# Kernel optimization log

Measured on AMD Instinct MI355X. Metric: run time of the kernel, lower is better.

The kernel has to match this reference:

```python
import jax, jax.numpy as jnp
import numpy as np
from jax.scipy.linalg import expm

D_LOGIC = 128
D_MEM = 16
SO_DIM = D_MEM * (D_MEM - 1) // 2  # 120


def _linear_init(key, fan_in, shape):
    bound = 1.0 / np.sqrt(fan_in)
    return jax.random.uniform(key, shape, jnp.float32, -bound, bound)


def setup_inputs() -> dict:
    key = jax.random.key(0)
    ks = jax.random.split(key, 14)
    B, S = 4, 128
    return {
        "x_logic": jax.random.normal(ks[0], (B, S, D_LOGIC), jnp.float32),
        "x_memory": jax.random.normal(ks[1], (B, S, D_MEM), jnp.float32),
        # W_Q / W_K
        "Wq": _linear_init(ks[2], D_LOGIC, (D_LOGIC, D_LOGIC)),
        "bq": _linear_init(ks[3], D_LOGIC, (D_LOGIC,)),
        "Wk": _linear_init(ks[4], D_LOGIC, (D_LOGIC, D_LOGIC)),
        "bk": _linear_init(ks[5], D_LOGIC, (D_LOGIC,)),
        # gamma_net: Linear(d_logic, 2*d_logic) -> Tanh -> Linear(2*d_logic, so_dim)
        "W1": _linear_init(ks[6], D_LOGIC, (2 * D_LOGIC, D_LOGIC)),
        "b1": _linear_init(ks[7], D_LOGIC, (2 * D_LOGIC,)),
        "W2": _linear_init(ks[8], 2 * D_LOGIC, (SO_DIM, 2 * D_LOGIC)),
        "b2": _linear_init(ks[9], 2 * D_LOGIC, (SO_DIM,)),
        # out_proj: Linear(d_memory, d_memory)
        "Wo": _linear_init(ks[10], D_MEM, (D_MEM, D_MEM)),
        "bo": _linear_init(ks[11], D_MEM, (D_MEM,)),
    }


def reference(x_logic, x_memory, Wq, bq, Wk, bk, W1, b1, W2, b2, Wo, bo):
    B, S, d_logic = x_logic.shape
    dm = x_memory.shape[-1]

    # attention over logic stream
    Q = x_logic @ Wq.T + bq
    K = x_logic @ Wk.T + bk
    attn = jax.nn.softmax(
        jnp.einsum("bjd,bid->bji", Q, K) / jnp.sqrt(jnp.float32(d_logic)), axis=-1
    )  # [B, S(j), S(i)]

    # per-pair Lie-algebra params: delta[b,j,i] = x_logic[b,j] - x_logic[b,i]
    delta = x_logic[:, :, None, :] - x_logic[:, None, :, :]  # [B,S,S,d_logic]
    h = jnp.tanh(delta @ W1.T + b1)
    lie = h @ W2.T + b2  # [B,S,S,so_dim]

    # scatter into skew-symmetric matrices [B,S,S,dm,dm]
    r, c = np.triu_indices(dm, k=1)
    skew = jnp.zeros((B, S, S, dm, dm), x_logic.dtype)
    skew = skew.at[..., r, c].set(lie)
    skew = skew.at[..., c, r].set(-lie)

    # Lie-group exponential -> orthogonal transport matrices
    T_all = expm(skew)  # [B,S,S,dm,dm]

    # transported[b,j,i,:] = T[b,j,i] @ x_memory[b,i]
    transported = jnp.einsum("bjide,bie->bjid", T_all, x_memory)

    # attention-weighted aggregation over i
    settled = jnp.einsum("bji,bjid->bjd", attn, transported)  # [B,S,dm]

    out = settled @ Wo.T + bo
    return out, T_all
```

## Files before the change

### kernel.cpp

```cpp
#include <hip/hip_runtime.h>
#include <hip/hip_fp16.h>

#define S_LEN 128
#define DLOG  128
#define DMEM  16
#define SO    120
#define HDIM  256

typedef _Float16 v8h __attribute__((ext_vector_type(8)));
typedef __fp16 v2hf __attribute__((ext_vector_type(2)));
typedef float v4f __attribute__((ext_vector_type(4)));

union PkU { v2hf h; unsigned u; };
union V8U { v8h v; int u[4]; };

__global__ __launch_bounds__(128) void qk_kernel(
    const float* __restrict__ xl, const float* __restrict__ Wq,
    const float* __restrict__ bq, const float* __restrict__ Wk,
    const float* __restrict__ bk, float* __restrict__ Q, float* __restrict__ K) {
  int bj = blockIdx.x, o = threadIdx.x;
  __shared__ float xs[128];
  xs[o] = xl[bj * 128 + o];
  __syncthreads();
  float aq = bq[o], ak = bk[o];
  const float* wq = Wq + o * 128;
  const float* wk = Wk + o * 128;
  #pragma unroll 4
  for (int d = 0; d < 128; ++d) {
    float x = xs[d];
    aq = fmaf(x, wq[d], aq);
    ak = fmaf(x, wk[d], ak);
  }
  Q[bj * 128 + o] = aq;
  K[bj * 128 + o] = ak;
}

__global__ __launch_bounds__(128) void attn_kernel(
    const float* __restrict__ Q, const float* __restrict__ K,
    float* __restrict__ attn) {
  int bj = blockIdx.x, b = bj >> 7, i = threadIdx.x;
  __shared__ float qs[128];
  __shared__ float red[128];
  qs[i] = Q[bj * 128 + i];
  __syncthreads();
  const float* kr = K + (b * 128 + i) * 128;
  float s = 0.f;
  #pragma unroll 4
  for (int d = 0; d < 128; ++d) s = fmaf(qs[d], kr[d], s);
  s *= 0.08838834764831845f;
  red[i] = s;
  __syncthreads();
  for (int off = 64; off; off >>= 1) {
    if (i < off) red[i] = fmaxf(red[i], red[i + off]);
    __syncthreads();
  }
  float m = red[0];
  __syncthreads();
  float e = expf(s - m);
  red[i] = e;
  __syncthreads();
  for (int off = 64; off; off >>= 1) {
    if (i < off) red[i] += red[i + off];
    __syncthreads();
  }
  attn[(size_t)bj * 128 + i] = e / red[0];
}

__global__ __launch_bounds__(256) void h_kernel(
    const float* __restrict__ xl, const float* __restrict__ W1,
    const float* __restrict__ b1, __half* __restrict__ hG) {
  __shared__ _Float16 w1s[128 * 136];
  __shared__ _Float16 dstage[64 * 136];
  __shared__ float xjs[128];
  int t = threadIdx.x;
  int blk = blockIdx.x;
  int bj = blk >> 1;
  int oh = blk & 1;
  int b = bj >> 7;
  int o0 = oh * 128;

  if (t < 128) xjs[t] = xl[bj * 128 + t];
  for (int idx = t; idx < 128 * 128; idx += 256) {
    int o = idx >> 7, k = idx & 127;
    w1s[o * 136 + k] = (_Float16)W1[(o0 + o) * 128 + k];
  }
  __syncthreads();

  int lane = t & 63, w = t >> 6;
  int nn = lane & 15, q = lane >> 4;
  int ow = o0 + w * 32;
  float bb0 = b1[ow + nn], bb1 = b1[ow + 16 + nn];
  const float* xb = xl + (size_t)b * 128 * 128;

  for (int pi = 0; pi < 2; ++pi) {
    for (int idx = t; idx < 64 * 128; idx += 256) {
      int i = idx >> 7, k = idx & 127;
      dstage[i * 136 + k] = (_Float16)(xjs[k] - xb[(pi * 64 + i) * 128 + k]);
    }
    __syncthreads();

    v4f acc[4][2];
    #pragma unroll
    for (int mi = 0; mi < 4; ++mi) {
      acc[mi][0] = (v4f){0.f, 0.f, 0.f, 0.f};
      acc[mi][1] = (v4f){0.f, 0.f, 0.f, 0.f};
    }
    #pragma unroll
    for (int ks = 0; ks < 4; ++ks) {
      v8h bf0 = *(const v8h*)&w1s[(w * 32 + nn) * 136 + ks * 32 + q * 8];
      v8h bf1 = *(const v8h*)&w1s[(w * 32 + 16 + nn) * 136 + ks * 32 + q * 8];
      #pragma unroll
      for (int mi = 0; mi < 4; ++mi) {
        v8h af = *(const v8h*)&dstage[(mi * 16 + nn) * 136 + ks * 32 + q * 8];
        acc[mi][0] = __builtin_amdgcn_mfma_f32_16x16x32_f16(af, bf0, acc[mi][0], 0, 0, 0);
        acc[mi][1] = __builtin_amdgcn_mfma_f32_16x16x32_f16(af, bf1, acc[mi][1], 0, 0, 0);
      }
    }
    #pragma unroll
    for (int mi = 0; mi < 4; ++mi) {
      #pragma unroll
      for (int nt = 0; nt < 2; ++nt) {
        int o = ow + nt * 16 + nn;
        float bbv = nt ? bb1 : bb0;
        #pragma unroll
        for (int reg = 0; reg < 4; ++reg) {
          int i = pi * 64 + mi * 16 + 4 * q + reg;
          float x = acc[mi][nt][reg] + bbv;
          float ax = fabsf(x);
          float e = __expf(-2.f * ax);
          float r = __fdividef(1.f - e, 1.f + e);
          r = copysignf(r, x);
          hG[(size_t)(bj * 128 + i) * 512 + o] = __float2half(r);
        }
      }
    }
    __syncthreads();
  }
}

__global__ __launch_bounds__(256) void lie_kernel(
    const float* __restrict__ W2g, const float* __restrict__ b2g,
    float* __restrict__ Tg) {
  __shared__ _Float16 w2t[128 * 136];
  int t = threadIdx.x, lane = t & 63;
  int wu = __builtin_amdgcn_readfirstlane(t >> 6);
  int pbase = blockIdx.x * 64 + wu * 16;
  int nn = lane & 15, q = lane >> 4;
  const _Float16* hf = (const _Float16*)Tg;

  v4f acc[8];
  #pragma unroll
  for (int tt = 0; tt < 8; ++tt) acc[tt] = (v4f){0.f, 0.f, 0.f, 0.f};

  const _Float16* hrow = hf + (size_t)(pbase + nn) * 512;
  for (int khalf = 0; khalf < 2; ++khalf) {
    __syncthreads();
    for (int idx = t; idx < 120 * 128; idx += 256) {
      int o = idx >> 7, kk = idx & 127;
      w2t[o * 136 + kk] = (_Float16)W2g[o * 256 + khalf * 128 + kk];
    }
    for (int idx = t; idx < 8 * 128; idx += 256)
      w2t[(120 + (idx >> 7)) * 136 + (idx & 127)] = (_Float16)0.f;
    __syncthreads();
    #pragma unroll
    for (int ks = 0; ks < 4; ++ks) {
      v8h ah = *(const v8h*)(hrow + khalf * 128 + ks * 32 + 8 * q);
      #pragma unroll
      for (int tt = 0; tt < 8; ++tt) {
        const v8h bf = *(const v8h*)(w2t + (16 * tt + nn) * 136 + ks * 32 + 8 * q);
        acc[tt] = __builtin_amdgcn_mfma_f32_16x16x32_f16(ah, bf, acc[tt], 0, 0, 0);
      }
    }
  }

  _Float16* hw = (_Float16*)Tg;
  #pragma unroll
  for (int tt = 0; tt < 8; ++tt) {
    int n16 = 16 * tt + nn;
    if (n16 < 120) {
      float bb = b2g[n16];
      #pragma unroll
      for (int reg = 0; reg < 4; ++reg) {
        size_t p = (size_t)(pbase + 4 * q + reg);
        hw[p * 512 + 256 + n16] = (_Float16)(acc[tt][reg] + bb);
      }
    }
  }
}

__device__ __forceinline__ void split8(const float* x, v8h& hi, v8h& lo) {
  union U { v8h v; v2hf p[4]; } H, L;
  #pragma unroll
  for (int i = 0; i < 4; ++i) {
    float a = x[2 * i], b = x[2 * i + 1];
    v2hf h = __builtin_amdgcn_cvt_pkrtz(a, b);
    float ra = (float)h[0], rb = (float)h[1];
    v2hf l = __builtin_amdgcn_cvt_pkrtz(a - ra, b - rb);
    H.p[i] = h;
    L.p[i] = l;
  }
  hi = H.v;
  lo = L.v;
}

__device__ __forceinline__ int lie_idx(int rr, int cc) {
  return 15 * rr - ((rr * (rr - 1)) >> 1) + cc - rr - 1;
}

__global__ __launch_bounds__(256) void expm_kernel(float* __restrict__ Tg) {
  __shared__ char lds[12288] __attribute__((aligned(16)));
  int t = threadIdx.x, lane = t & 63;
  int wu = __builtin_amdgcn_readfirstlane(t >> 6);
  int pbase = blockIdx.x * 8 + wu * 2;
  int nn = lane & 15, q = lane >> 4, b8 = (q & 1) * 8;
  char* wb = lds + wu * 3072;
  _Float16* lieS = (_Float16*)wb;
  float* ErB = (float*)(wb + 512);
  const _Float16* hf = (const _Float16*)Tg;

  int idxA = ((2 * (q & 1)) * 16 + nn) * 4;
  int idxB = idxA + 64;

  float scv[2];
  int sv[2];
  #pragma unroll
  for (int j = 0; j < 2; ++j) {
    size_t p = (size_t)(pbase + j);
    _Float16 a0 = (lane < 120) ? hf[p * 512 + 256 + lane] : (_Float16)0.f;
    _Float16 a1 = (lane < 56) ? hf[p * 512 + 320 + lane] : (_Float16)0.f;
    lieS[j * 128 + lane] = a0;
    lieS[j * 128 + 64 + lane] = a1;
    float f0 = (float)a0, f1 = (float)a1;
    float s2 = f0 * f0 + f1 * f1;
    #pragma unroll
    for (int off = 1; off < 64; off <<= 1) s2 += __shfl_xor(s2, off, 64);
    float bound = sqrtf(s2);
    int s = 0;
    while (bound > 1.0f && s < 12) { bound *= 0.5f; s++; }
    sv[j] = __builtin_amdgcn_readfirstlane(s);
    scv[j] = ldexpf(1.0f, -s);
  }
  asm volatile("s_waitcnt lgkmcnt(0)" ::: "memory");

  V8U Apk[2], bf[2];
  v4f E[2];
  #pragma unroll
  for (int j = 0; j < 2; ++j) {
    const _Float16* lp = lieS + j * 128;
    float sc = scv[j];
    float av[8];
    #pragma unroll
    for (int jj = 0; jj < 8; ++jj) {
      int c = b8 + jj;
      int rr = min(nn, c), c2 = max(nn, c);
      float lv = (c == nn) ? 0.f : (float)lp[lie_idx(rr, c2)];
      av[jj] = (c == nn) ? 0.f : ((c > nn) ? lv : -lv) * sc;
    }
    #pragma unroll
    for (int i = 0; i < 4; ++i) {
      PkU u;
      u.h = __builtin_amdgcn_cvt_pkrtz(av[2 * i], av[2 * i + 1]);
      Apk[j].u[i] = (int)u.u;
    }
    #pragma unroll
    for (int i = 0; i < 4; ++i) bf[j].u[i] = Apk[j].u[i] ^ 0x80008000;
    #pragma unroll
    for (int reg = 0; reg < 4; ++reg) {
      int r = 4 * q + reg;
      int rr = min(r, nn), c2 = max(r, nn);
      float lv = (r == nn) ? 0.f : (float)lp[lie_idx(rr, c2)];
      float v = (r == nn) ? 0.f : ((nn > r) ? lv : -lv) * sc;
      E[j][reg] = v + ((r == nn) ? 1.f : 0.f);
    }
  }

  #pragma unroll
  for (int k = 2; k <= 9; ++k) {
    const float rk = 1.0f / (2.0f * (float)k);
    #pragma unroll
    for (int j = 0; j < 2; ++j) {
      v4f z = {0.f, 0.f, 0.f, 0.f};
      v4f c4 = __builtin_amdgcn_mfma_f32_16x16x32_f16(Apk[j].v, bf[j].v, z, 0, 0, 0);
      c4 = c4 * rk;
      E[j] += c4;
      if (k < 9) {
        PkU u0, u1;
        u0.h = __builtin_amdgcn_cvt_pkrtz(c4[0], c4[1]);
        u1.h = __builtin_amdgcn_cvt_pkrtz(c4[2], c4[3]);
        bf[j].u[0] = __builtin_amdgcn_ds_bpermute(idxA, (int)u0.u);
        bf[j].u[1] = __builtin_amdgcn_ds_bpermute(idxA, (int)u1.u);
        bf[j].u[2] = __builtin_amdgcn_ds_bpermute(idxB, (int)u0.u);
        bf[j].u[3] = __builtin_amdgcn_ds_bpermute(idxB, (int)u1.u);
      }
    }
  }

  int smax = max(sv[0], sv[1]);
  for (int it = 0; it < smax; ++it) {
    #pragma unroll
    for (int j = 0; j < 2; ++j) {
      if (it < sv[j]) {
        float* Erp = ErB + j * 320;
        PkU u0, u1;
        u0.h = __builtin_amdgcn_cvt_pkrtz(E[j][0], E[j][1]);
        u1.h = __builtin_amdgcn_cvt_pkrtz(E[j][2], E[j][3]);
        V8U bfe;
        bfe.u[0] = __builtin_amdgcn_ds_bpermute(idxA, (int)u0.u);
        bfe.u[1] = __builtin_amdgcn_ds_bpermute(idxA, (int)u1.u);
        bfe.u[2] = __builtin_amdgcn_ds_bpermute(idxB, (int)u0.u);
        bfe.u[3] = __builtin_amdgcn_ds_bpermute(idxB, (int)u1.u);
        #pragma unroll
        for (int reg = 0; reg < 4; ++reg)
          Erp[(4 * q + reg) * 20 + nn] = E[j][reg];
        asm volatile("s_waitcnt lgkmcnt(0)" ::: "memory");
        float4 a0 = *(const float4*)(Erp + nn * 20 + b8);
        float4 a1 = *(const float4*)(Erp + nn * 20 + b8 + 4);
        float xa[8] = {a0.x, a0.y, a0.z, a0.w, a1.x, a1.y, a1.z, a1.w};
        v8h ahi, alo;
        split8(xa, ahi, alo);
        v8h Ecat = (q < 2) ? ahi : alo;
        v4f z = {0.f, 0.f, 0.f, 0.f};
        E[j] = __builtin_amdgcn_mfma_f32_16x16x32_f16(Ecat, bfe.v, z, 0, 0, 0);
      }
    }
  }

  #pragma unroll
  for (int j = 0; j < 2; ++j) {
    float* dst = Tg + (size_t)(pbase + j) * 256;
    #pragma unroll
    for (int reg = 0; reg < 4; ++reg)
      dst[(4 * q + reg) * 16 + nn] = E[j][reg];
  }
}

__global__ __launch_bounds__(256) void settle_kernel(
    const float* __restrict__ Tg, const float* __restrict__ attn,
    const float* __restrict__ xm, const float* __restrict__ Wo,
    const float* __restrict__ bo, float* __restrict__ outp) {
  int bj = blockIdx.x, b = bj >> 7;
  int t = threadIdx.x, lane = t & 63;
  int wu = __builtin_amdgcn_readfirstlane(t >> 6);
  int r = lane >> 2, a = lane & 3;
  float pacc = 0.f;
  for (int ii = 0; ii < 32; ++ii) {
    int i = wu * 32 + ii;
    size_t p = (size_t)bj * 128 + i;
    const float4 tv = *(const float4*)(Tg + (p << 8) + lane * 4);
    const float* xv = xm + (b * 128 + i) * 16;
    float aw = attn[p];
    float y = tv.x * xv[4 * a] + tv.y * xv[4 * a + 1] +
              tv.z * xv[4 * a + 2] + tv.w * xv[4 * a + 3];
    y += __shfl_xor(y, 1, 64);
    y += __shfl_xor(y, 2, 64);
    pacc = fmaf(aw, y, pacc);
  }
  __shared__ float sred[4][16];
  __shared__ float sfin[16];
  if (a == 0) sred[wu][r] = pacc;
  __syncthreads();
  if (t < 16) sfin[t] = sred[0][t] + sred[1][t] + sred[2][t] + sred[3][t];
  __syncthreads();
  if (t < 16) {
    float o = bo[t];
    const float* wr = Wo + t * 16;
    #pragma unroll
    for (int c = 0; c < 16; c++) o = fmaf(wr[c], sfin[c], o);
    outp[bj * 16 + t] = o;
  }
}

extern "C" void kernel_launch(void* const* d_in, const int* in_sizes, int n_in,
                              void* d_out, int out_size, void* d_ws,
                              size_t ws_size, hipStream_t stream) {
  const float* xl = (const float*)d_in[0];
  const float* xm = (const float*)d_in[1];
  const float* Wq = (const float*)d_in[2];
  const float* bq = (const float*)d_in[3];
  const float* Wk = (const float*)d_in[4];
  const float* bk = (const float*)d_in[5];
  const float* W1 = (const float*)d_in[6];
  const float* b1 = (const float*)d_in[7];
  const float* W2 = (const float*)d_in[8];
  const float* b2 = (const float*)d_in[9];
  const float* Wo = (const float*)d_in[10];
  const float* bo = (const float*)d_in[11];
  float* outp = (float*)d_out;
  float* Tg = outp + 8192;
  float* wsf = (float*)d_ws;
  float* Q = wsf;
  float* K = wsf + 65536;
  float* attn = wsf + 131072;

  hipLaunchKernelGGL(qk_kernel, dim3(512), dim3(128), 0, stream, xl, Wq, bq, Wk, bk, Q, K);
  hipLaunchKernelGGL(attn_kernel, dim3(512), dim3(128), 0, stream, Q, K, attn);
  hipLaunchKernelGGL(h_kernel, dim3(1024), dim3(256), 0, stream, xl, W1, b1, (__half*)Tg);
  hipLaunchKernelGGL(lie_kernel, dim3(1024), dim3(256), 0, stream, W2, b2, Tg);
  hipLaunchKernelGGL(expm_kernel, dim3(8192), dim3(256), 0, stream, Tg);
  hipLaunchKernelGGL(settle_kernel, dim3(512), dim3(256), 0, stream, Tg, attn, xm, Wo, bo, outp);
}
```

Baseline: 218.6 us.

## Evaluate Taylor expm via Paterson-Stockmeyer and fuse settle reduction into expm

The sequential degree-9 Taylor recurrence (eight dependent MFMAs per pair) becomes a Paterson-Stockmeyer style polynomial built from A, A^2, A^4 and a few combining MFMAs, which shortens the dependent chain. It also exploits A^T = -A by using negated-A fragments. The attention-weighted transport reduction moves from a separate settle kernel that reread all of T into the expm epilogue, which writes per-block partial sums, and a small final kernel applies the output projection. The polynomial coefficients are folded into fp16 operands, which may change numerical accuracy.

```diff
diff --git a/kernel.cpp b/kernel.cpp
--- a/kernel.cpp
+++ b/kernel.cpp
@@ -13,6 +13,12 @@
 
 union PkU { v2hf h; unsigned u; };
 union V8U { v8h v; int u[4]; };
+
+__device__ __forceinline__ v8h splat8(float x) {
+  _Float16 h = (_Float16)x;
+  v8h v = {h, h, h, h, h, h, h, h};
+  return v;
+}
 
 __global__ __launch_bounds__(128) void qk_kernel(
     const float* __restrict__ xl, const float* __restrict__ Wq,
@@ -207,8 +213,11 @@
   return 15 * rr - ((rr * (rr - 1)) >> 1) + cc - rr - 1;
 }
 
-__global__ __launch_bounds__(256) void expm_kernel(float* __restrict__ Tg) {
+__global__ __launch_bounds__(256) void expm_kernel(
+    float* __restrict__ Tg, const float* __restrict__ attn,
+    const float* __restrict__ xm, float* __restrict__ part) {
   __shared__ char lds[12288] __attribute__((aligned(16)));
+  __shared__ float sred[4][16];
   int t = threadIdx.x, lane = t & 63;
   int wu = __builtin_amdgcn_readfirstlane(t >> 6);
   int pbase = blockIdx.x * 8 + wu * 2;
@@ -242,8 +251,8 @@
   }
   asm volatile("s_waitcnt lgkmcnt(0)" ::: "memory");
 
-  V8U Apk[2], bf[2];
-  v4f E[2];
+  V8U Apk[2], BfA[2];
+  v4f Af[2];
   #pragma unroll
   for (int j = 0; j < 2; ++j) {
     const _Float16* lp = lieS + j * 128;
@@ -261,38 +270,107 @@
       PkU u;
       u.h = __builtin_amdgcn_cvt_pkrtz(av[2 * i], av[2 * i + 1]);
       Apk[j].u[i] = (int)u.u;
-    }
-    #pragma unroll
-    for (int i = 0; i < 4; ++i) bf[j].u[i] = Apk[j].u[i] ^ 0x80008000;
+      BfA[j].u[i] = Apk[j].u[i] ^ 0x80008000;
+    }
     #pragma unroll
     for (int reg = 0; reg < 4; ++reg) {
       int r = 4 * q + reg;
       int rr = min(r, nn), c2 = max(r, nn);
       float lv = (r == nn) ? 0.f : (float)lp[lie_idx(rr, c2)];
-      float v = (r == nn) ? 0.f : ((nn > r) ? lv : -lv) * sc;
-      E[j][reg] = v + ((r == nn) ? 1.f : 0.f);
-    }
-  }
-
-  #pragma unroll
-  for (int k = 2; k <= 9; ++k) {
-    const float rk = 1.0f / (2.0f * (float)k);
-    #pragma unroll
-    for (int j = 0; j < 2; ++j) {
-      v4f z = {0.f, 0.f, 0.f, 0.f};
-      v4f c4 = __builtin_amdgcn_mfma_f32_16x16x32_f16(Apk[j].v, bf[j].v, z, 0, 0, 0);
-      c4 = c4 * rk;
-      E[j] += c4;
-      if (k < 9) {
-        PkU u0, u1;
-        u0.h = __builtin_amdgcn_cvt_pkrtz(c4[0], c4[1]);
-        u1.h = __builtin_amdgcn_cvt_pkrtz(c4[2], c4[3]);
-        bf[j].u[0] = __builtin_amdgcn_ds_bpermute(idxA, (int)u0.u);
-        bf[j].u[1] = __builtin_amdgcn_ds_bpermute(idxA, (int)u1.u);
-        bf[j].u[2] = __builtin_amdgcn_ds_bpermute(idxB, (int)u0.u);
-        bf[j].u[3] = __builtin_amdgcn_ds_bpermute(idxB, (int)u1.u);
-      }
-    }
+      Af[j][reg] = (r == nn) ? 0.f : ((nn > r) ? lv : -lv) * sc;
+    }
+  }
+
+  V8U IC1, IC2;
+  #pragma unroll
+  for (int i = 0; i < 4; ++i) {
+    float d0 = (b8 + 2 * i == nn) ? 1.f : 0.f;
+    float d1 = (b8 + 2 * i + 1 == nn) ? 1.f : 0.f;
+    PkU u1, u2;
+    u1.h = __builtin_amdgcn_cvt_pkrtz(10.666667f * d0, 10.666667f * d1);
+    u2.h = __builtin_amdgcn_cvt_pkrtz(2.1333333f * d0, 2.1333333f * d1);
+    IC1.u[i] = (int)u1.u;
+    IC2.u[i] = (int)u2.u;
+  }
+
+  v4f z4 = {0.f, 0.f, 0.f, 0.f};
+
+  v4f cB[2];
+  #pragma unroll
+  for (int j = 0; j < 2; ++j)
+    cB[j] = __builtin_amdgcn_mfma_f32_16x16x32_f16(Apk[j].v, BfA[j].v, z4, 0, 0, 0);
+
+  V8U fB[2];
+  #pragma unroll
+  for (int j = 0; j < 2; ++j) {
+    PkU u0, u1;
+    u0.h = __builtin_amdgcn_cvt_pkrtz(cB[j][0], cB[j][1]);
+    u1.h = __builtin_amdgcn_cvt_pkrtz(cB[j][2], cB[j][3]);
+    fB[j].u[0] = __builtin_amdgcn_ds_bpermute(idxA, (int)u0.u);
+    fB[j].u[1] = __builtin_amdgcn_ds_bpermute(idxA, (int)u1.u);
+    fB[j].u[2] = __builtin_amdgcn_ds_bpermute(idxB, (int)u0.u);
+    fB[j].u[3] = __builtin_amdgcn_ds_bpermute(idxB, (int)u1.u);
+  }
+
+  v4f cB2[2];
+  #pragma unroll
+  for (int j = 0; j < 2; ++j)
+    cB2[j] = __builtin_amdgcn_mfma_f32_16x16x32_f16(fB[j].v, fB[j].v, z4, 0, 0, 0);
+
+  V8U fB2[2];
+  #pragma unroll
+  for (int j = 0; j < 2; ++j) {
+    PkU u0, u1;
+    u0.h = __builtin_amdgcn_cvt_pkrtz(cB2[j][0], cB2[j][1]);
+    u1.h = __builtin_amdgcn_cvt_pkrtz(cB2[j][2], cB2[j][3]);
+    fB2[j].u[0] = __builtin_amdgcn_ds_bpermute(idxA, (int)u0.u);
+    fB2[j].u[1] = __builtin_amdgcn_ds_bpermute(idxA, (int)u1.u);
+    fB2[j].u[2] = __builtin_amdgcn_ds_bpermute(idxB, (int)u0.u);
+    fB2[j].u[3] = __builtin_amdgcn_ds_bpermute(idxB, (int)u1.u);
+  }
+
+  v8h k1a = splat8(7.9365079e-4f);
+  v8h k1b = splat8(0.17777778f);
+  v8h k2a = splat8(8.8183422e-5f);
+  v8h k2b = splat8(2.5396825e-2f);
+  V8U M1[2], M2[2];
+  #pragma unroll
+  for (int j = 0; j < 2; ++j) {
+    M1[j].v = fB2[j].v * k1a + (fB[j].v * k1b + IC1.v);
+    M2[j].v = fB2[j].v * k2a + (fB[j].v * k2b + IC2.v);
+  }
+
+  v4f Cc[2], Qc[2];
+  #pragma unroll
+  for (int j = 0; j < 2; ++j) {
+    v4f c3m = __builtin_amdgcn_mfma_f32_16x16x32_f16(M1[j].v, fB2[j].v, z4, 0, 0, 0);
+    v4f c4m = __builtin_amdgcn_mfma_f32_16x16x32_f16(M2[j].v, fB2[j].v, z4, 0, 0, 0);
+    #pragma unroll
+    for (int reg = 0; reg < 4; ++reg) {
+      float dg = (4 * q + reg == nn) ? 1.f : 0.f;
+      Cc[j][reg] = fmaf(c3m[reg], 2.44140625e-4f,
+                        fmaf(cB[j][reg], 0.25f, dg + Af[j][reg]));
+      Qc[j][reg] = fmaf(c4m[reg], 2.44140625e-4f, cB[j][reg] * 0.083333333f);
+    }
+  }
+
+  V8U fQ[2];
+  #pragma unroll
+  for (int j = 0; j < 2; ++j) {
+    PkU u0, u1;
+    u0.h = __builtin_amdgcn_cvt_pkrtz(Qc[j][0], Qc[j][1]);
+    u1.h = __builtin_amdgcn_cvt_pkrtz(Qc[j][2], Qc[j][3]);
+    fQ[j].u[0] = __builtin_amdgcn_ds_bpermute(idxA, (int)u0.u);
+    fQ[j].u[1] = __builtin_amdgcn_ds_bpermute(idxA, (int)u1.u);
+    fQ[j].u[2] = __builtin_amdgcn_ds_bpermute(idxB, (int)u0.u);
+    fQ[j].u[3] = __builtin_amdgcn_ds_bpermute(idxB, (int)u1.u);
+  }
+
+  v4f E[2];
+  #pragma unroll
+  for (int j = 0; j < 2; ++j) {
+    v4f c5 = __builtin_amdgcn_mfma_f32_16x16x32_f16(Apk[j].v, fQ[j].v, z4, 0, 0, 0);
+    E[j] = Cc[j] + c5 * 0.5f;
   }
 
   int smax = max(sv[0], sv[1]);
@@ -325,47 +403,55 @@
     }
   }
 
-  #pragma unroll
-  for (int j = 0; j < 2; ++j) {
-    float* dst = Tg + (size_t)(pbase + j) * 256;
+  float pacc[4] = {0.f, 0.f, 0.f, 0.f};
+  #pragma unroll
+  for (int j = 0; j < 2; ++j) {
+    int p = pbase + j;
+    float* dst = Tg + (size_t)p * 256;
     #pragma unroll
     for (int reg = 0; reg < 4; ++reg)
       dst[(4 * q + reg) * 16 + nn] = E[j][reg];
-  }
-}
-
-__global__ __launch_bounds__(256) void settle_kernel(
-    const float* __restrict__ Tg, const float* __restrict__ attn,
-    const float* __restrict__ xm, const float* __restrict__ Wo,
+    int b = p >> 14, i = p & 127;
+    float xv = xm[((b << 7) + i) * 16 + nn];
+    float aw = attn[(size_t)p] * xv;
+    #pragma unroll
+    for (int reg = 0; reg < 4; ++reg)
+      pacc[reg] = fmaf(aw, E[j][reg], pacc[reg]);
+  }
+  #pragma unroll
+  for (int reg = 0; reg < 4; ++reg) {
+    #pragma unroll
+    for (int off = 1; off < 16; off <<= 1)
+      pacc[reg] += __shfl_xor(pacc[reg], off, 64);
+  }
+  if (nn == 0) {
+    #pragma unroll
+    for (int reg = 0; reg < 4; ++reg) sred[wu][4 * q + reg] = pacc[reg];
+  }
+  __syncthreads();
+  if (t < 16)
+    part[(size_t)blockIdx.x * 16 + t] =
+        sred[0][t] + sred[1][t] + sred[2][t] + sred[3][t];
+}
+
+__global__ __launch_bounds__(64) void settle_fin_kernel(
+    const float* __restrict__ part, const float* __restrict__ Wo,
     const float* __restrict__ bo, float* __restrict__ outp) {
-  int bj = blockIdx.x, b = bj >> 7;
-  int t = threadIdx.x, lane = t & 63;
-  int wu = __builtin_amdgcn_readfirstlane(t >> 6);
-  int r = lane >> 2, a = lane & 3;
-  float pacc = 0.f;
-  for (int ii = 0; ii < 32; ++ii) {
-    int i = wu * 32 + ii;
-    size_t p = (size_t)bj * 128 + i;
-    const float4 tv = *(const float4*)(Tg + (p << 8) + lane * 4);
-    const float* xv = xm + (b * 128 + i) * 16;
-    float aw = attn[p];
-    float y = tv.x * xv[4 * a] + tv.y * xv[4 * a + 1] +
-              tv.z * xv[4 * a + 2] + tv.w * xv[4 * a + 3];
-    y += __shfl_xor(y, 1, 64);
-    y += __shfl_xor(y, 2, 64);
-    pacc = fmaf(aw, y, pacc);
-  }
-  __shared__ float sred[4][16];
-  __shared__ float sfin[16];
-  if (a == 0) sred[wu][r] = pacc;
-  __syncthreads();
-  if (t < 16) sfin[t] = sred[0][t] + sred[1][t] + sred[2][t] + sred[3][t];
+  int bj = blockIdx.x, t = threadIdx.x;
+  int r = t & 15, e0 = t >> 4;
+  const float* pb = part + (size_t)bj * 256;
+  float s = pb[e0 * 16 + r] + pb[(e0 + 4) * 16 + r] +
+            pb[(e0 + 8) * 16 + r] + pb[(e0 + 12) * 16 + r];
+  __shared__ float sf[64];
+  sf[t] = s;
+  __syncthreads();
+  if (t < 16) sf[t] = sf[t] + sf[16 + t] + sf[32 + t] + sf[48 + t];
   __syncthreads();
   if (t < 16) {
     float o = bo[t];
     const float* wr = Wo + t * 16;
     #pragma unroll
-    for (int c = 0; c < 16; c++) o = fmaf(wr[c], sfin[c], o);
+    for (int c = 0; c < 16; ++c) o = fmaf(wr[c], sf[c], o);
     outp[bj * 16 + t] = o;
   }
 }
@@ -391,11 +477,12 @@
   float* Q = wsf;
   float* K = wsf + 65536;
   float* attn = wsf + 131072;
+  float* part = wsf + 196608;
 
   hipLaunchKernelGGL(qk_kernel, dim3(512), dim3(128), 0, stream, xl, Wq, bq, Wk, bk, Q, K);
   hipLaunchKernelGGL(attn_kernel, dim3(512), dim3(128), 0, stream, Q, K, attn);
   hipLaunchKernelGGL(h_kernel, dim3(1024), dim3(256), 0, stream, xl, W1, b1, (__half*)Tg);
   hipLaunchKernelGGL(lie_kernel, dim3(1024), dim3(256), 0, stream, W2, b2, Tg);
-  hipLaunchKernelGGL(expm_kernel, dim3(8192), dim3(256), 0, stream, Tg);
-  hipLaunchKernelGGL(settle_kernel, dim3(512), dim3(256), 0, stream, Tg, attn, xm, Wo, bo, outp);
-}
+  hipLaunchKernelGGL(expm_kernel, dim3(8192), dim3(256), 0, stream, Tg, attn, xm, part);
+  hipLaunchKernelGGL(settle_fin_kernel, dim3(512), dim3(64), 0, stream, part, Wo, bo, outp);
+}
```

New measurement: 206.6 us. -5.5%, faster.
